# Kernel tuning notes

Hardware: AMD Instinct MI355X
Metric: run time of the kernel (lower is better)

The kernel has to match this reference:

```python
import jax, jax.numpy as jnp
import numpy as np

NEG_SLOPE = 0.2  # PyG GATConv default negative_slope


def gat_layer(x, src, dst, W, a_src, a_dst, bias, concat, N):
    """PyG GATConv: h = xW; e_ij = LeakyReLU(a_src.h_j + a_dst.h_i);
    alpha = segment-softmax over incoming edges of i; out_i = sum_j alpha_ij h_j."""
    H, C = a_src.shape
    h = (x @ W).reshape(N, H, C)                      # [N,H,C]
    alpha_s = jnp.einsum('nhc,hc->nh', h, a_src)      # [N,H]
    alpha_d = jnp.einsum('nhc,hc->nh', h, a_dst)      # [N,H]
    e = jax.nn.leaky_relu(alpha_s[src] + alpha_d[dst], NEG_SLOPE)  # [E,H]
    # numerically-stable segment softmax over destination nodes
    m = jax.ops.segment_max(e, dst, num_segments=N)   # [N,H]
    e = jnp.exp(e - m[dst])
    denom = jax.ops.segment_sum(e, dst, num_segments=N)
    alpha = e / (denom[dst] + 1e-16)                  # [E,H]
    msg = h[src] * alpha[:, :, None]                  # [E,H,C]
    out = jax.ops.segment_sum(msg, dst, num_segments=N)  # [N,H,C]
    out = out.reshape(N, H * C) if concat else out.mean(axis=1)
    return out + bias


def setup_inputs() -> dict:
    key = jax.random.key(0)
    ks = jax.random.split(key, 12)
    N, E, F_IN, C, H = 50000, 800000, 512, 32, 8
    s = 0.05
    x = jax.random.normal(ks[0], (N, F_IN), dtype=jnp.float32)
    edge_index = jax.random.randint(ks[1], (2, E), 0, N, dtype=jnp.int64)
    W1 = jax.random.normal(ks[2], (F_IN, H * C), dtype=jnp.float32) * s
    as1 = jax.random.normal(ks[3], (H, C), dtype=jnp.float32) * s
    ad1 = jax.random.normal(ks[4], (H, C), dtype=jnp.float32) * s
    b1 = jnp.zeros((H * C,), dtype=jnp.float32)
    W2 = jax.random.normal(ks[5], (H * C, H * C), dtype=jnp.float32) * s
    as2 = jax.random.normal(ks[6], (H, C), dtype=jnp.float32) * s
    ad2 = jax.random.normal(ks[7], (H, C), dtype=jnp.float32) * s
    b2 = jnp.zeros((C,), dtype=jnp.float32)
    Wp = jax.random.normal(ks[8], (C, 1), dtype=jnp.float32) * s
    bp = jnp.zeros((1,), dtype=jnp.float32)
    return {"edge_index": edge_index, "x": x, "W1": W1, "as1": as1, "ad1": ad1,
            "b1": b1, "W2": W2, "as2": as2, "ad2": ad2, "b2": b2,
            "Wp": Wp, "bp": bp}


def reference(edge_index, x, W1, as1, ad1, b1, W2, as2, ad2, b2, Wp, bp):
    N = x.shape[0]
    # PyG GATConv adds self-loops by default
    loops = jnp.arange(N, dtype=edge_index.dtype)
    src = jnp.concatenate([edge_index[0], loops])
    dst = jnp.concatenate([edge_index[1], loops])
    h = gat_layer(x, src, dst, W1, as1, ad1, b1, concat=True, N=N)
    h = jax.nn.relu(h)
    # F.dropout(training=self.training) is identity in eval mode
    h = gat_layer(h, src, dst, W2, as2, ad2, b2, concat=False, N=N)
    return jax.nn.sigmoid(h @ Wp + bp)   # [N,1]
```

## Files before the change

kernel.cpp:

```cpp
#include <hip/hip_runtime.h>
#include <math.h>

#define H_HEADS 8
#define C_DIM   32
#define HC      256
#define F_IN    512
#define NEG_SLOPE 0.2f

typedef __attribute__((ext_vector_type(8))) short    bf16x8;
typedef __attribute__((ext_vector_type(4))) short    s16x4;
typedef __attribute__((ext_vector_type(4))) float    f32x4;
typedef __attribute__((ext_vector_type(2))) float    f32x2;
typedef __attribute__((ext_vector_type(8))) _Float16 h16x8;

__device__ __forceinline__ short f2bf(float f) {
    union { float f; unsigned u; } v; v.f = f;
    unsigned r = v.u + 0x7FFF + ((v.u >> 16) & 1);
    return (short)(r >> 16);
}

__device__ __forceinline__ void gl2lds16(const short* g, short* l) {
    __builtin_amdgcn_global_load_lds(
        (const __attribute__((address_space(1))) void*)g,
        (__attribute__((address_space(3))) void*)l, 16, 0, 0);
}

__global__ void wfrag_kernel(const float* __restrict__ W, short* __restrict__ Wf, int K)
{
    int tid = blockIdx.x * 256 + threadIdx.x;
    if (tid >= K * HC) return;
    int j  = tid & 7;
    int l  = (tid >> 3) & 63;
    int nb = (tid >> 9) & 15;
    int s  = tid >> 13;
    int k  = s * 32 + (l >> 4) * 8 + j;
    int n  = nb * 16 + (l & 15);
    Wf[tid] = f2bf(W[(size_t)k * HC + n]);
}

template<bool ABF16>
__global__ __launch_bounds__(256) void gemm_mfma(const void* __restrict__ Aptr,
    const short* __restrict__ Bf, unsigned char* __restrict__ h8,
    const float* __restrict__ a_s, const float* __restrict__ a_d,
    float* __restrict__ alpha_s, float* __restrict__ alpha_d, int M, int K)
{
    __shared__ short Bs[2][8192];
    __shared__ float Als[512], Ald[512];

    const int tid  = threadIdx.x;
    const int w    = tid >> 6;
    const int lane = tid & 63;
    const int quad = lane >> 4;
    const int ml   = lane & 15;
    const int bm   = blockIdx.x * 64;

    const int rowA = bm + w * 16 + ml;
    const int rowL = rowA < M ? rowA : M - 1;

    f32x4 acc[16];
    #pragma unroll
    for (int nb = 0; nb < 16; ++nb) acc[nb] = (f32x4){0.f, 0.f, 0.f, 0.f};

    const float* A32 = (const float*)Aptr;
    const short* A16 = (const short*)Aptr;
    const int nsteps = K >> 5;

    {
        const short* g = Bf + (size_t)w * 2048 + lane * 8;
        short* l = &Bs[0][w * 2048];
        #pragma unroll
        for (int c = 0; c < 4; ++c) gl2lds16(g + c * 512, l + c * 512);
    }

    float4 p0, p1;
    bf16x8 pb;
    if (ABF16) {
        pb = *(const bf16x8*)(A16 + (size_t)rowL * K + quad * 8);
    } else {
        const float* ap = A32 + (size_t)rowL * K + quad * 8;
        p0 = *(const float4*)(ap);
        p1 = *(const float4*)(ap + 4);
    }

    for (int s = 0; s < nsteps; ++s) {
        __syncthreads();

        if (s + 1 < nsteps) {
            const short* g = Bf + (size_t)(s + 1) * 8192 + w * 2048 + lane * 8;
            short* l = &Bs[(s + 1) & 1][w * 2048];
            #pragma unroll
            for (int c = 0; c < 4; ++c) gl2lds16(g + c * 512, l + c * 512);
        }

        bf16x8 af;
        if (ABF16) {
            af = pb;
            if (s + 1 < nsteps)
                pb = *(const bf16x8*)(A16 + (size_t)rowL * K + (s + 1) * 32 + quad * 8);
        } else {
            af[0] = f2bf(p0.x); af[1] = f2bf(p0.y); af[2] = f2bf(p0.z); af[3] = f2bf(p0.w);
            af[4] = f2bf(p1.x); af[5] = f2bf(p1.y); af[6] = f2bf(p1.z); af[7] = f2bf(p1.w);
            if (s + 1 < nsteps) {
                const float* ap = A32 + (size_t)rowL * K + (s + 1) * 32 + quad * 8;
                p0 = *(const float4*)(ap);
                p1 = *(const float4*)(ap + 4);
            }
        }

        const short* bsrc = &Bs[s & 1][lane * 8];
        #pragma unroll
        for (int nb = 0; nb < 16; ++nb) {
            bf16x8 bfr = *(const bf16x8*)(bsrc + nb * 512);
            acc[nb] = __builtin_amdgcn_mfma_f32_16x16x32_bf16(af, bfr, acc[nb], 0, 0, 0);
        }
    }

    float as_v[16], ad_v[16];
    #pragma unroll
    for (int nb = 0; nb < 16; ++nb) {
        as_v[nb] = a_s[nb * 16 + ml];
        ad_v[nb] = a_d[nb * 16 + ml];
    }

    #pragma unroll
    for (int r = 0; r < 4; ++r) {
        const int rl  = w * 16 + quad * 4 + r;
        const int row = bm + rl;

        if (row < M) {
            unsigned char* hrow = h8 + (size_t)row * HC;
            #pragma unroll
            for (int i = 0; i < 8; ++i) {
                int pk = __builtin_amdgcn_cvt_pk_fp8_f32(acc[2 * i][r], acc[2 * i + 1][r], 0, false);
                hrow[(2 * i) * 16 + ml]     = (unsigned char)(pk & 0xFF);
                hrow[(2 * i + 1) * 16 + ml] = (unsigned char)((pk >> 8) & 0xFF);
            }
        }

        float hs[8], hd[8];
        #pragma unroll
        for (int q = 0; q < 8; ++q) {
            hs[q] = acc[2 * q][r] * as_v[2 * q] + acc[2 * q + 1][r] * as_v[2 * q + 1];
            hd[q] = acc[2 * q][r] * ad_v[2 * q] + acc[2 * q + 1][r] * ad_v[2 * q + 1];
        }
        #pragma unroll
        for (int off = 1; off < 16; off <<= 1) {
            #pragma unroll
            for (int q = 0; q < 8; ++q) {
                hs[q] += __shfl_xor(hs[q], off);
                hd[q] += __shfl_xor(hd[q], off);
            }
        }
        if (ml == 0) {
            #pragma unroll
            for (int q = 0; q < 8; ++q) {
                Als[rl * 8 + q] = hs[q];
                Ald[rl * 8 + q] = hd[q];
            }
        }
    }
    __syncthreads();
    #pragma unroll
    for (int k = 0; k < 2; ++k) {
        int idx = tid + k * 256;
        int rl = idx >> 3, q = idx & 7;
        int row = bm + rl;
        if (row < M) {
            alpha_s[(size_t)row * H_HEADS + q] = Als[idx];
            alpha_d[(size_t)row * H_HEADS + q] = Ald[idx];
        }
    }
}

__global__ __launch_bounds__(256) void wcalc_kernel(const int2* __restrict__ es,
    const float* __restrict__ alpha_s, const float* __restrict__ alpha_d,
    _Float16* __restrict__ wq, int P)
{
    int p = blockIdx.x * 256 + threadIdx.x;
    if (p >= P) return;
    int2 sd = es[p];
    const float4* as = (const float4*)(alpha_s + (size_t)sd.x * H_HEADS);
    const float4* ad = (const float4*)(alpha_d + (size_t)sd.y * H_HEADS);
    float4 s0 = as[0], s1 = as[1], d0 = ad[0], d1 = ad[1];
    float e[8] = {s0.x + d0.x, s0.y + d0.y, s0.z + d0.z, s0.w + d0.w,
                  s1.x + d1.x, s1.y + d1.y, s1.z + d1.z, s1.w + d1.w};
    h16x8 o;
    #pragma unroll
    for (int h = 0; h < 8; ++h) {
        float v = e[h] > 0.f ? e[h] : NEG_SLOPE * e[h];
        o[h] = (_Float16)__expf(v);
    }
    *(h16x8*)(wq + (size_t)p * H_HEADS) = o;
}

__global__ void zero_int(int* __restrict__ p, int n)
{
    int i = blockIdx.x * 256 + threadIdx.x;
    if (i < n) p[i] = 0;
}

__global__ void hist_kernel(const int* __restrict__ ei, int E, int N,
                            int* __restrict__ cnt)
{
    int e = blockIdx.x * 256 + threadIdx.x;
    if (e < E) atomicAdd(&cnt[ei[E + e]], 1);
    else if (e < E + N) atomicAdd(&cnt[e - E], 1);
}

__global__ __launch_bounds__(256) void scan_sum(const int* __restrict__ cnt, int n,
                                                int* __restrict__ chunk_sum)
{
    __shared__ int lds[256];
    int b = blockIdx.x, t = threadIdx.x;
    int base = b * 1024 + t * 4;
    int s = 0;
    #pragma unroll
    for (int j = 0; j < 4; ++j) { int i = base + j; if (i < n) s += cnt[i]; }
    lds[t] = s; __syncthreads();
    for (int off = 128; off > 0; off >>= 1) {
        if (t < off) lds[t] += lds[t + off];
        __syncthreads();
    }
    if (t == 0) chunk_sum[b] = lds[0];
}

__global__ void scan_top(const int* __restrict__ chunk_sum, int nch,
                         int* __restrict__ chunk_off, int* __restrict__ row_ptr,
                         int n_nodes)
{
    int t = threadIdx.x;
    int v = (t < nch) ? chunk_sum[t] : 0;
    int inc = v;
    #pragma unroll
    for (int off = 1; off < 64; off <<= 1) {
        int u = __shfl_up(inc, off);
        if (t >= off) inc += u;
    }
    if (t < nch) chunk_off[t] = inc - v;
    if (t == 63) row_ptr[n_nodes] = inc;
}

__global__ __launch_bounds__(256) void scan_local(const int* __restrict__ cnt, int n,
    const int* __restrict__ chunk_off, int* __restrict__ row_ptr)
{
    __shared__ int lds[256];
    int b = blockIdx.x, t = threadIdx.x;
    int base = b * 1024 + t * 4;
    int v[4]; int s = 0;
    #pragma unroll
    for (int j = 0; j < 4; ++j) { int i = base + j; v[j] = (i < n) ? cnt[i] : 0; s += v[j]; }
    lds[t] = s; __syncthreads();
    for (int off = 1; off < 256; off <<= 1) {
        int u = (t >= off) ? lds[t - off] : 0;
        __syncthreads();
        lds[t] += u;
        __syncthreads();
    }
    int run = lds[t] - s + chunk_off[b];
    #pragma unroll
    for (int j = 0; j < 4; ++j) {
        int i = base + j;
        if (i < n) row_ptr[i] = run;
        run += v[j];
    }
}

__global__ void scatter_kernel(const int* __restrict__ ei, int E, int N,
    const int* __restrict__ row_ptr, int* __restrict__ fill, int2* __restrict__ es)
{
    int e = blockIdx.x * 256 + threadIdx.x;
    int src, dst;
    if (e < E)          { src = ei[e]; dst = ei[E + e]; }
    else if (e < E + N) { src = dst = e - E; }
    else return;
    int pos = row_ptr[dst] + atomicAdd(&fill[dst], 1);
    es[pos] = make_int2(src, dst);
}

__global__ __launch_bounds__(256) void agg1_kernel(const unsigned* __restrict__ h8,
    const _Float16* __restrict__ wq, const int* __restrict__ row_ptr,
    const int2* __restrict__ es, const float* __restrict__ bias,
    short* __restrict__ z_bf, int N)
{
    const int l = threadIdx.x & 63;
    const int i = blockIdx.x * 4 + (threadIdx.x >> 6);
    if (i >= N) return;
    const int hh = l >> 3;
    const int beg = row_ptr[i], end = row_ptr[i + 1];
    f32x4 acc = {0.f, 0.f, 0.f, 0.f};
    float dsum = 0.f;
    int p = beg;
    for (; p + 7 < end; p += 8) {
        int s[8]; float w[8]; unsigned hv[8];
        #pragma unroll
        for (int u = 0; u < 8; ++u) s[u] = es[p + u].x;
        #pragma unroll
        for (int u = 0; u < 8; ++u) w[u] = (float)wq[(size_t)(p + u) * 8 + hh];
        #pragma unroll
        for (int u = 0; u < 8; ++u) hv[u] = h8[(size_t)s[u] * 64 + l];
        #pragma unroll
        for (int u = 0; u < 8; ++u) {
            f32x2 lo = __builtin_amdgcn_cvt_pk_f32_fp8(hv[u], false);
            f32x2 hi = __builtin_amdgcn_cvt_pk_f32_fp8(hv[u], true);
            acc[0] = fmaf(w[u], lo[0], acc[0]);
            acc[1] = fmaf(w[u], lo[1], acc[1]);
            acc[2] = fmaf(w[u], hi[0], acc[2]);
            acc[3] = fmaf(w[u], hi[1], acc[3]);
            dsum += w[u];
        }
    }
    for (; p < end; ++p) {
        int s0 = es[p].x;
        float w0 = (float)wq[(size_t)p * 8 + hh];
        unsigned hv = h8[(size_t)s0 * 64 + l];
        f32x2 lo = __builtin_amdgcn_cvt_pk_f32_fp8(hv, false);
        f32x2 hi = __builtin_amdgcn_cvt_pk_f32_fp8(hv, true);
        acc[0] = fmaf(w0, lo[0], acc[0]);
        acc[1] = fmaf(w0, lo[1], acc[1]);
        acc[2] = fmaf(w0, hi[0], acc[2]);
        acc[3] = fmaf(w0, hi[1], acc[3]);
        dsum += w0;
    }
    float inv = 1.f / (dsum + 1e-16f);
    s16x4 pk;
    #pragma unroll
    for (int j = 0; j < 4; ++j) {
        float z = acc[j] * inv + bias[4 * l + j];
        pk[j] = f2bf(z > 0.f ? z : 0.f);
    }
    *(s16x4*)(z_bf + (size_t)i * HC + 4 * l) = pk;
}

__global__ __launch_bounds__(256) void agg2_kernel(const unsigned* __restrict__ h8,
    const _Float16* __restrict__ wq, const int* __restrict__ row_ptr,
    const int2* __restrict__ es, const float* __restrict__ b2,
    const float* __restrict__ Wp, const float* __restrict__ bp,
    float* __restrict__ out, int N)
{
    const int l = threadIdx.x & 63;
    const int i = blockIdx.x * 4 + (threadIdx.x >> 6);
    if (i >= N) return;
    const int hh = l >> 3;
    const int beg = row_ptr[i], end = row_ptr[i + 1];
    f32x4 acc = {0.f, 0.f, 0.f, 0.f};
    float dsum = 0.f;
    int p = beg;
    for (; p + 7 < end; p += 8) {
        int s[8]; float w[8]; unsigned hv[8];
        #pragma unroll
        for (int u = 0; u < 8; ++u) s[u] = es[p + u].x;
        #pragma unroll
        for (int u = 0; u < 8; ++u) w[u] = (float)wq[(size_t)(p + u) * 8 + hh];
        #pragma unroll
        for (int u = 0; u < 8; ++u) hv[u] = h8[(size_t)s[u] * 64 + l];
        #pragma unroll
        for (int u = 0; u < 8; ++u) {
            f32x2 lo = __builtin_amdgcn_cvt_pk_f32_fp8(hv[u], false);
            f32x2 hi = __builtin_amdgcn_cvt_pk_f32_fp8(hv[u], true);
            acc[0] = fmaf(w[u], lo[0], acc[0]);
            acc[1] = fmaf(w[u], lo[1], acc[1]);
            acc[2] = fmaf(w[u], hi[0], acc[2]);
            acc[3] = fmaf(w[u], hi[1], acc[3]);
            dsum += w[u];
        }
    }
    for (; p < end; ++p) {
        int s0 = es[p].x;
        float w0 = (float)wq[(size_t)p * 8 + hh];
        unsigned hv = h8[(size_t)s0 * 64 + l];
        f32x2 lo = __builtin_amdgcn_cvt_pk_f32_fp8(hv, false);
        f32x2 hi = __builtin_amdgcn_cvt_pk_f32_fp8(hv, true);
        acc[0] = fmaf(w0, lo[0], acc[0]);
        acc[1] = fmaf(w0, lo[1], acc[1]);
        acc[2] = fmaf(w0, hi[0], acc[2]);
        acc[3] = fmaf(w0, hi[1], acc[3]);
        dsum += w0;
    }
    float inv = 1.f / (dsum + 1e-16f);
    int cc = (4 * l) & 31;
    float partial = 0.f;
    #pragma unroll
    for (int j = 0; j < 4; ++j) partial = fmaf(acc[j] * inv, Wp[cc + j], partial);
    if (l < 8) {
        #pragma unroll
        for (int j = 0; j < 4; ++j) partial = fmaf(8.f * b2[4 * l + j], Wp[4 * l + j], partial);
    }
    #pragma unroll
    for (int off = 32; off > 0; off >>= 1) partial += __shfl_xor(partial, off);
    if (l == 0) out[i] = 1.f / (1.f + __expf(-(0.125f * partial + bp[0])));
}

extern "C" void kernel_launch(void* const* d_in, const int* in_sizes, int n_in,
                              void* d_out, int out_size, void* d_ws, size_t ws_size,
                              hipStream_t stream)
{
    const int*   ei  = (const int*)d_in[0];
    const float* x   = (const float*)d_in[1];
    const float* W1  = (const float*)d_in[2];
    const float* as1 = (const float*)d_in[3];
    const float* ad1 = (const float*)d_in[4];
    const float* b1  = (const float*)d_in[5];
    const float* W2  = (const float*)d_in[6];
    const float* as2 = (const float*)d_in[7];
    const float* ad2 = (const float*)d_in[8];
    const float* b2  = (const float*)d_in[9];
    const float* Wp  = (const float*)d_in[10];
    const float* bp  = (const float*)d_in[11];
    float* out = (float*)d_out;

    const int E = in_sizes[0] / 2;
    const int N = in_sizes[1] / F_IN;
    const int ET = E + N;

    float*         asb = (float*)d_ws;
    float*         adb = asb + (size_t)N * H_HEADS;
    unsigned char* h8  = (unsigned char*)(adb + (size_t)N * H_HEADS);
    short*         z1b = (short*)(h8 + (size_t)N * HC);
    short*         Wf1 = z1b + (size_t)N * HC;
    short*         Wf2 = Wf1 + (size_t)F_IN * HC;
    _Float16*      wq  = (_Float16*)(Wf2 + (size_t)HC * HC);
    int2*          es  = (int2*)(wq + (size_t)ET * H_HEADS);
    int* cnt       = (int*)(es + ET);
    int* fill      = cnt + N;
    int* row_ptr   = fill + N;
    int* chunk_off = row_ptr + N + 1;
    int* chunk_sum = chunk_off + 64;

    const int NCH = (N + 1023) / 1024;
    const int MB  = (N + 63) / 64;
    const int NB4 = (N + 3) / 4;

    zero_int<<<(2 * N + 255) / 256, 256, 0, stream>>>(cnt, 2 * N);
    hist_kernel<<<(ET + 255) / 256, 256, 0, stream>>>(ei, E, N, cnt);
    scan_sum<<<NCH, 256, 0, stream>>>(cnt, N, chunk_sum);
    scan_top<<<1, 64, 0, stream>>>(chunk_sum, NCH, chunk_off, row_ptr, N);
    scan_local<<<NCH, 256, 0, stream>>>(cnt, N, chunk_off, row_ptr);
    scatter_kernel<<<(ET + 255) / 256, 256, 0, stream>>>(ei, E, N, row_ptr, fill, es);

    wfrag_kernel<<<(F_IN * HC + 255) / 256, 256, 0, stream>>>(W1, Wf1, F_IN);
    wfrag_kernel<<<(HC * HC + 255) / 256, 256, 0, stream>>>(W2, Wf2, HC);

    gemm_mfma<false><<<MB, 256, 0, stream>>>(x, Wf1, h8, as1, ad1, asb, adb, N, F_IN);
    wcalc_kernel<<<(ET + 255) / 256, 256, 0, stream>>>(es, asb, adb, wq, ET);
    agg1_kernel<<<NB4, 256, 0, stream>>>((const unsigned*)h8, wq, row_ptr, es, b1, z1b, N);

    gemm_mfma<true><<<MB, 256, 0, stream>>>(z1b, Wf2, h8, as2, ad2, asb, adb, N, HC);
    wcalc_kernel<<<(ET + 255) / 256, 256, 0, stream>>>(es, asb, adb, wq, ET);
    agg2_kernel<<<NB4, 256, 0, stream>>>((const unsigned*)h8, wq, row_ptr, es, b2, Wp, bp, out, N);
}
```

Before: 423.2 us.

## Split GEMMs into specialized kernels, persistent layer-2 GEMM, two-pass CSR scatter

The layer-1 GEMM is specialised to fp32 input with a two-step-deep register prefetch of A. It reuses the B LDS buffer for the alpha reduction and sets an occupancy hint. Layer 2 now uses a persistent kernel that keeps half of the bf16 W2 fragments resident in LDS per block and loops over row tiles, splitting the output columns across block pairs. The CSR scatter becomes two passes: a coarse bucket by 64-node groups using global atomics, then an in-block pass using LDS atomics, to cut global atomic contention. The cost is an extra temp edge buffer and one more kernel launch.

```diff
diff --git a/kernel.cpp b/kernel.cpp
--- a/kernel.cpp
+++ b/kernel.cpp
@@ -38,14 +38,12 @@
     Wf[tid] = f2bf(W[(size_t)k * HC + n]);
 }
 
-template<bool ABF16>
-__global__ __launch_bounds__(256) void gemm_mfma(const void* __restrict__ Aptr,
+__global__ __launch_bounds__(256, 4) void gemm1_mfma(const float* __restrict__ A32,
     const short* __restrict__ Bf, unsigned char* __restrict__ h8,
     const float* __restrict__ a_s, const float* __restrict__ a_d,
-    float* __restrict__ alpha_s, float* __restrict__ alpha_d, int M, int K)
+    float* __restrict__ alpha_s, float* __restrict__ alpha_d, int M)
 {
     __shared__ short Bs[2][8192];
-    __shared__ float Als[512], Ald[512];
 
     const int tid  = threadIdx.x;
     const int w    = tid >> 6;
@@ -61,9 +59,7 @@
     #pragma unroll
     for (int nb = 0; nb < 16; ++nb) acc[nb] = (f32x4){0.f, 0.f, 0.f, 0.f};
 
-    const float* A32 = (const float*)Aptr;
-    const short* A16 = (const short*)Aptr;
-    const int nsteps = K >> 5;
+    const int nsteps = F_IN >> 5;
 
     {
         const short* g = Bf + (size_t)w * 2048 + lane * 8;
@@ -72,15 +68,12 @@
         for (int c = 0; c < 4; ++c) gl2lds16(g + c * 512, l + c * 512);
     }
 
-    float4 p0, p1;
-    bf16x8 pb;
-    if (ABF16) {
-        pb = *(const bf16x8*)(A16 + (size_t)rowL * K + quad * 8);
-    } else {
-        const float* ap = A32 + (size_t)rowL * K + quad * 8;
-        p0 = *(const float4*)(ap);
-        p1 = *(const float4*)(ap + 4);
-    }
+    const float* abase = A32 + (size_t)rowL * F_IN + quad * 8;
+    float4 pa[2][2];
+    pa[0][0] = *(const float4*)(abase);
+    pa[0][1] = *(const float4*)(abase + 4);
+    pa[1][0] = *(const float4*)(abase + 32);
+    pa[1][1] = *(const float4*)(abase + 36);
 
     for (int s = 0; s < nsteps; ++s) {
         __syncthreads();
@@ -93,18 +86,14 @@
         }
 
         bf16x8 af;
-        if (ABF16) {
-            af = pb;
-            if (s + 1 < nsteps)
-                pb = *(const bf16x8*)(A16 + (size_t)rowL * K + (s + 1) * 32 + quad * 8);
-        } else {
-            af[0] = f2bf(p0.x); af[1] = f2bf(p0.y); af[2] = f2bf(p0.z); af[3] = f2bf(p0.w);
-            af[4] = f2bf(p1.x); af[5] = f2bf(p1.y); af[6] = f2bf(p1.z); af[7] = f2bf(p1.w);
-            if (s + 1 < nsteps) {
-                const float* ap = A32 + (size_t)rowL * K + (s + 1) * 32 + quad * 8;
-                p0 = *(const float4*)(ap);
-                p1 = *(const float4*)(ap + 4);
-            }
+        {
+            float4 q0 = pa[s & 1][0], q1 = pa[s & 1][1];
+            af[0] = f2bf(q0.x); af[1] = f2bf(q0.y); af[2] = f2bf(q0.z); af[3] = f2bf(q0.w);
+            af[4] = f2bf(q1.x); af[5] = f2bf(q1.y); af[6] = f2bf(q1.z); af[7] = f2bf(q1.w);
+        }
+        if (s + 2 < nsteps) {
+            pa[s & 1][0] = *(const float4*)(abase + (s + 2) * 32);
+            pa[s & 1][1] = *(const float4*)(abase + (s + 2) * 32 + 4);
         }
 
         const short* bsrc = &Bs[s & 1][lane * 8];
@@ -121,6 +110,10 @@
         as_v[nb] = a_s[nb * 16 + ml];
         ad_v[nb] = a_d[nb * 16 + ml];
     }
+
+    __syncthreads();
+    float* Als = (float*)&Bs[0][0];
+    float* Ald = Als + 512;
 
     #pragma unroll
     for (int r = 0; r < 4; ++r) {
@@ -168,6 +161,102 @@
         if (row < M) {
             alpha_s[(size_t)row * H_HEADS + q] = Als[idx];
             alpha_d[(size_t)row * H_HEADS + q] = Ald[idx];
+        }
+    }
+}
+
+__global__ __launch_bounds__(256) void gemm2_persist(const short* __restrict__ z1b,
+    const short* __restrict__ Bf2, unsigned char* __restrict__ h8,
+    const float* __restrict__ a_s, const float* __restrict__ a_d,
+    float* __restrict__ alpha_s, float* __restrict__ alpha_d, int M)
+{
+    __shared__ short Bs[32768];
+
+    const int tid  = threadIdx.x;
+    const int w    = tid >> 6;
+    const int lane = tid & 63;
+    const int quad = lane >> 4;
+    const int ml   = lane & 15;
+    const int ch   = blockIdx.x & 1;
+    const int bid2 = blockIdx.x >> 1;
+    const int bstr = gridDim.x >> 1;
+
+    #pragma unroll
+    for (int s = 0; s < 8; ++s) {
+        const short* gbase = Bf2 + (size_t)(s * 16 + ch * 8) * 512;
+        #pragma unroll
+        for (int sw = 0; sw < 2; ++sw) {
+            int i = sw * 2048 + tid * 8;
+            gl2lds16(gbase + i, &Bs[s * 4096 + i]);
+        }
+    }
+    __syncthreads();
+
+    float as_v[8], ad_v[8];
+    #pragma unroll
+    for (int nb = 0; nb < 8; ++nb) {
+        as_v[nb] = a_s[(ch * 8 + nb) * 16 + ml];
+        ad_v[nb] = a_d[(ch * 8 + nb) * 16 + ml];
+    }
+
+    const int nt = (M + 63) >> 6;
+    for (int rt = bid2; rt < nt; rt += bstr) {
+        const int rowA = rt * 64 + w * 16 + ml;
+        const int rowL = rowA < M ? rowA : M - 1;
+        const short* arow = z1b + (size_t)rowL * HC;
+
+        bf16x8 av[8];
+        #pragma unroll
+        for (int s = 0; s < 8; ++s)
+            av[s] = *(const bf16x8*)(arow + s * 32 + quad * 8);
+
+        f32x4 acc[8];
+        #pragma unroll
+        for (int nb = 0; nb < 8; ++nb) acc[nb] = (f32x4){0.f, 0.f, 0.f, 0.f};
+
+        #pragma unroll
+        for (int s = 0; s < 8; ++s) {
+            const short* bsrc = &Bs[s * 4096 + lane * 8];
+            #pragma unroll
+            for (int nb = 0; nb < 8; ++nb) {
+                bf16x8 bfr = *(const bf16x8*)(bsrc + nb * 512);
+                acc[nb] = __builtin_amdgcn_mfma_f32_16x16x32_bf16(av[s], bfr, acc[nb], 0, 0, 0);
+            }
+        }
+
+        #pragma unroll
+        for (int r = 0; r < 4; ++r) {
+            const int row = rt * 64 + w * 16 + quad * 4 + r;
+            float hs[4], hd[4];
+            #pragma unroll
+            for (int q = 0; q < 4; ++q) {
+                hs[q] = acc[2 * q][r] * as_v[2 * q] + acc[2 * q + 1][r] * as_v[2 * q + 1];
+                hd[q] = acc[2 * q][r] * ad_v[2 * q] + acc[2 * q + 1][r] * ad_v[2 * q + 1];
+            }
+            #pragma unroll
+            for (int off = 1; off < 16; off <<= 1) {
+                #pragma unroll
+                for (int q = 0; q < 4; ++q) {
+                    hs[q] += __shfl_xor(hs[q], off);
+                    hd[q] += __shfl_xor(hd[q], off);
+                }
+            }
+            if (row < M) {
+                unsigned char* hrow = h8 + (size_t)row * HC;
+                #pragma unroll
+                for (int i = 0; i < 4; ++i) {
+                    int pk = __builtin_amdgcn_cvt_pk_fp8_f32(acc[2 * i][r], acc[2 * i + 1][r], 0, false);
+                    hrow[(ch * 8 + 2 * i) * 16 + ml]     = (unsigned char)(pk & 0xFF);
+                    hrow[(ch * 8 + 2 * i + 1) * 16 + ml] = (unsigned char)((pk >> 8) & 0xFF);
+                }
+                if (ml == 0) {
+                    #pragma unroll
+                    for (int q = 0; q < 4; ++q) {
+                        alpha_s[(size_t)row * H_HEADS + ch * 4 + q] = hs[q];
+                        alpha_d[(size_t)row * H_HEADS + ch * 4 + q] = hd[q];
+                    }
+                }
+            }
         }
     }
 }
@@ -265,16 +354,34 @@
     }
 }
 
-__global__ void scatter_kernel(const int* __restrict__ ei, int E, int N,
-    const int* __restrict__ row_ptr, int* __restrict__ fill, int2* __restrict__ es)
+__global__ void scatter1_kernel(const int* __restrict__ ei, int E, int N,
+    const int* __restrict__ row_ptr, int* __restrict__ fill1, int2* __restrict__ tmp)
 {
     int e = blockIdx.x * 256 + threadIdx.x;
     int src, dst;
     if (e < E)          { src = ei[e]; dst = ei[E + e]; }
     else if (e < E + N) { src = dst = e - E; }
     else return;
-    int pos = row_ptr[dst] + atomicAdd(&fill[dst], 1);
-    es[pos] = make_int2(src, dst);
+    int b = dst >> 6;
+    int pos = row_ptr[b << 6] + atomicAdd(&fill1[b], 1);
+    tmp[pos] = make_int2(src, dst);
+}
+
+__global__ __launch_bounds__(256) void scatter2_kernel(const int2* __restrict__ tmp,
+    const int* __restrict__ row_ptr, int N, int2* __restrict__ es)
+{
+    __shared__ int f[64];
+    int b = blockIdx.x;
+    int n0 = b * 64;
+    int n1 = n0 + 64; if (n1 > N) n1 = N;
+    if (threadIdx.x < 64) f[threadIdx.x] = 0;
+    __syncthreads();
+    int p0 = row_ptr[n0], p1 = row_ptr[n1];
+    for (int p = p0 + threadIdx.x; p < p1; p += 256) {
+        int2 sd = tmp[p];
+        int pos = row_ptr[sd.y] + atomicAdd(&f[sd.y & 63], 1);
+        es[pos] = sd;
+    }
 }
 
 __global__ __launch_bounds__(256) void agg1_kernel(const unsigned* __restrict__ h8,
@@ -408,9 +515,10 @@
     const float* bp  = (const float*)d_in[11];
     float* out = (float*)d_out;
 
-    const int E = in_sizes[0] / 2;
-    const int N = in_sizes[1] / F_IN;
-    const int ET = E + N;
+    const int E   = in_sizes[0] / 2;
+    const int N   = in_sizes[1] / F_IN;
+    const int ET  = E + N;
+    const int NBK = (N + 63) / 64;
 
     float*         asb = (float*)d_ws;
     float*         adb = asb + (size_t)N * H_HEADS;
@@ -420,9 +528,10 @@
     short*         Wf2 = Wf1 + (size_t)F_IN * HC;
     _Float16*      wq  = (_Float16*)(Wf2 + (size_t)HC * HC);
     int2*          es  = (int2*)(wq + (size_t)ET * H_HEADS);
-    int* cnt       = (int*)(es + ET);
-    int* fill      = cnt + N;
-    int* row_ptr   = fill + N;
+    int2*          tmp = es + ET;
+    int* cnt       = (int*)(tmp + ET);
+    int* fill1     = cnt + N;
+    int* row_ptr   = fill1 + NBK;
     int* chunk_off = row_ptr + N + 1;
     int* chunk_sum = chunk_off + 64;
 
@@ -430,21 +539,22 @@
     const int MB  = (N + 63) / 64;
     const int NB4 = (N + 3) / 4;
 
-    zero_int<<<(2 * N + 255) / 256, 256, 0, stream>>>(cnt, 2 * N);
+    zero_int<<<(N + NBK + 255) / 256, 256, 0, stream>>>(cnt, N + NBK);
     hist_kernel<<<(ET + 255) / 256, 256, 0, stream>>>(ei, E, N, cnt);
     scan_sum<<<NCH, 256, 0, stream>>>(cnt, N, chunk_sum);
     scan_top<<<1, 64, 0, stream>>>(chunk_sum, NCH, chunk_off, row_ptr, N);
     scan_local<<<NCH, 256, 0, stream>>>(cnt, N, chunk_off, row_ptr);
-    scatter_kernel<<<(ET + 255) / 256, 256, 0, stream>>>(ei, E, N, row_ptr, fill, es);
+    scatter1_kernel<<<(ET + 255) / 256, 256, 0, stream>>>(ei, E, N, row_ptr, fill1, tmp);
+    scatter2_kernel<<<NBK, 256, 0, stream>>>(tmp, row_ptr, N, es);
 
     wfrag_kernel<<<(F_IN * HC + 255) / 256, 256, 0, stream>>>(W1, Wf1, F_IN);
     wfrag_kernel<<<(HC * HC + 255) / 256, 256, 0, stream>>>(W2, Wf2, HC);
 
-    gemm_mfma<false><<<MB, 256, 0, stream>>>(x, Wf1, h8, as1, ad1, asb, adb, N, F_IN);
+    gemm1_mfma<<<MB, 256, 0, stream>>>(x, Wf1, h8, as1, ad1, asb, adb, N);
     wcalc_kernel<<<(ET + 255) / 256, 256, 0, stream>>>(es, asb, adb, wq, ET);
     agg1_kernel<<<NB4, 256, 0, stream>>>((const unsigned*)h8, wq, row_ptr, es, b1, z1b, N);
 
-    gemm_mfma<true><<<MB, 256, 0, stream>>>(z1b, Wf2, h8, as2, ad2, asb, adb, N, HC);
+    gemm2_persist<<<512, 256, 0, stream>>>(z1b, Wf2, h8, as2, ad2, asb, adb, N);
     wcalc_kernel<<<(ET + 255) / 256, 256, 0, stream>>>(es, asb, adb, wq, ET);
     agg2_kernel<<<NB4, 256, 0, stream>>>((const unsigned*)h8, wq, row_ptr, es, b2, Wp, bp, out, N);
 }
```

Measured after the change: 632.3 us. 1.49x slower.
